# Kernel tuning notes

Measured on AMD Instinct MI355X. Metric: run time of the kernel, lower is better.

The kernel has to match this reference:

```python
import jax, jax.numpy as jnp
import numpy as np

B, T, V, E, H = 64, 512, 32000, 256, 512


def setup_inputs() -> dict:
    key = jax.random.key(0)
    k0, k1, k2, k3 = jax.random.split(key, 4)
    sequence_input = jax.random.randint(k0, (B, T), 0, V)
    emb_table = jax.random.normal(k1, (V, E), dtype=jnp.float32) * 0.02
    Wx = jax.random.normal(k2, (E, 4 * H), dtype=jnp.float32) * (1.0 / np.sqrt(E))
    Wh = jax.random.normal(k3, (H, 4 * H), dtype=jnp.float32) * (1.0 / np.sqrt(H))
    # Keras unit_forget_bias=True: forget-gate bias initialized to 1
    b = jnp.zeros((4 * H,), dtype=jnp.float32).at[H:2 * H].set(1.0)
    return {"sequence_input": sequence_input, "emb_table": emb_table,
            "Wx": Wx, "Wh": Wh, "b": b}


def _lstm(xz, Wh):
    # xz: [T, B, 4H] precomputed input projections (+bias); scan the recurrence.
    h0 = jnp.zeros((xz.shape[1], H), dtype=xz.dtype)
    c0 = jnp.zeros_like(h0)

    def step(carry, z_t):
        h, c = carry
        z = z_t + h @ Wh                      # [B, 4H]
        i, f, g, o = jnp.split(z, 4, axis=-1)  # Keras gate order: i, f, c(g), o
        i = jax.nn.sigmoid(i)
        f = jax.nn.sigmoid(f)
        g = jnp.tanh(g)
        o = jax.nn.sigmoid(o)
        c = f * c + i * g
        h = o * jnp.tanh(c)
        return (h, c), h

    (h_last, _c), seq = jax.lax.scan(step, (h0, c0), xz)
    return seq, h_last


def reference(sequence_input, emb_table, Wx, Wh, b):
    x = emb_table[sequence_input]                     # [B, T, E]
    xz = jnp.einsum('bte,eg->btg', x, Wx) + b         # [B, T, 4H]
    seq, h_last = _lstm(jnp.swapaxes(xz, 0, 1), Wh)   # seq: [T, B, H]
    seq = jnp.swapaxes(seq, 0, 1)                     # [B, T, H]
    mask = (sequence_input != 0).astype(jnp.float32)[..., None]  # [B, T, 1]
    return seq, h_last, mask
```

## Files before the change

kernel.cpp:

```cpp
#include <hip/hip_runtime.h>
#include <stdint.h>

#define B_   64
#define T_   512
#define E_   256
#define H_   512
#define G4_  2048
#define V_   32000

#define OUT_SEQ   0
#define OUT_HLAST 16777216
#define OUT_MASK  16809984

#define OFF_EMB  0u
#define OFF_WXT  16384000u
#define OFF_WHT  17432576u
#define OFF_C    19529728u
#define OFF_XZ   19660800u
#define XZ_PER_T   262144u
#define RING_PER_T  65536u
#define SLOT_U64    8192


#define POISON64 0xFFFFFFFFFFFFFFFFULL

typedef short bf16x8 __attribute__((ext_vector_type(8)));
typedef float f32x4  __attribute__((ext_vector_type(4)));
typedef unsigned int u32x4 __attribute__((ext_vector_type(4)));

__device__ __forceinline__ unsigned short f2bf(float f) {
  uint32_t u = __float_as_uint(f);
  u = (u + 0x7FFFu + ((u >> 16) & 1u)) >> 16;
  return (unsigned short)u;
}
__device__ __forceinline__ float bf2f(unsigned short h) {
  return __uint_as_float(((uint32_t)h) << 16);
}
__device__ __forceinline__ float sigmoid_f(float x) {
  return __fdividef(1.f, 1.f + __expf(-x));
}
__device__ __forceinline__ float tanh_f(float x) {
  return 1.f - __fdividef(2.f, 1.f + __expf(2.f * x));
}

__global__ void k_prep_emb(const float* __restrict__ emb, unsigned short* __restrict__ out) {
  int i = (blockIdx.x * 256 + threadIdx.x) * 4;
  if (i < V_ * E_) {
    float4 v = *(const float4*)(emb + i);
    ushort4 o;
    o.x = f2bf(v.x); o.y = f2bf(v.y); o.z = f2bf(v.z); o.w = f2bf(v.w);
    *(ushort4*)(out + i) = o;
  }
}

__global__ void k_prep_w(const float* __restrict__ Wx, const float* __restrict__ Wh,
                         unsigned short* __restrict__ wxt, unsigned short* __restrict__ wht) {
  int i = blockIdx.x * 256 + threadIdx.x;
  if (i < 524288) {
    int n = i >> 8, k = i & 255;
    wxt[i] = f2bf(Wx[k * G4_ + n]);
  } else if (i < 524288 + 1048576) {
    int j = i - 524288;
    int n = j >> 9, k = j & 511;
    wht[j] = f2bf(Wh[k * G4_ + n]);
  }
}

__global__ void k_mask(const int* __restrict__ seq, float* __restrict__ out) {
  int i = blockIdx.x * 256 + threadIdx.x;
  if (i < B_ * T_) out[OUT_MASK + i] = (seq[i] != 0) ? 1.f : 0.f;
}

__global__ __launch_bounds__(256) void k_copyseq(const unsigned int* __restrict__ ring,
                                                 float* __restrict__ out, int t0, int R) {
  int t = t0 + blockIdx.x;
  const unsigned int* src = ring + (size_t)(t % R) * (SLOT_U64 * 2);
  for (int i = threadIdx.x; i < B_ * H_ / 2; i += 256) {
    int b = i >> 8;
    int j = (i & 255) * 2;
    unsigned int v = src[((((b >> 4) * 64 + (j >> 3)) * 16 + (b & 15)) * 4) + ((j >> 1) & 3)];
    float2 o;
    o.x = bf2f((unsigned short)(v & 0xFFFFu));
    o.y = bf2f((unsigned short)(v >> 16));
    *(float2*)(out + ((size_t)b * T_ + t) * H_ + j) = o;
  }
}

__global__ void k_hlast(const unsigned int* __restrict__ ring, float* __restrict__ out, int R) {
  int i = blockIdx.x * 256 + threadIdx.x;
  if (i < B_ * H_) {
    int b = i >> 9, j = i & 511;
    unsigned int v = ring[(size_t)((T_ - 1) % R) * (SLOT_U64 * 2) +
                          ((((b >> 4) * 64 + (j >> 3)) * 16 + (b & 15)) * 4) + ((j >> 1) & 3)];
    out[OUT_HLAST + i] = bf2f((unsigned short)((j & 1) ? (v >> 16) : (v & 0xFFFFu)));
  }
}

#define LDA_ 264
__global__ __launch_bounds__(256) void k_gemm_xz(
    const int* __restrict__ seq, const unsigned short* __restrict__ embb,
    const unsigned short* __restrict__ wxt, const float* __restrict__ bias,
    unsigned short* __restrict__ xz, int t0) {
  __shared__ __align__(16) unsigned short a_lds[128 * LDA_];
  __shared__ __align__(16) unsigned short b_lds[128 * LDA_];
  int bx = blockIdx.x & 15;
  int by = blockIdx.x >> 4;
  int tid = threadIdx.x;

  {
    int r = tid >> 1, half = tid & 1;
    int m = by * 128 + r;
    int t = t0 + (m >> 6), b = m & 63;
    int idx = seq[b * T_ + t];
    const unsigned short* srcA = embb + (size_t)idx * E_ + half * 128;
    const unsigned short* srcB = wxt + (size_t)(bx * 128 + r) * E_ + half * 128;
    unsigned short* dstA = a_lds + r * LDA_ + half * 128;
    unsigned short* dstB = b_lds + r * LDA_ + half * 128;
#pragma unroll
    for (int q = 0; q < 16; ++q) {
      *(bf16x8*)(dstA + q * 8) = *(const bf16x8*)(srcA + q * 8);
      *(bf16x8*)(dstB + q * 8) = *(const bf16x8*)(srcB + q * 8);
    }
  }
  __syncthreads();

  int w = tid >> 6, lane = tid & 63;
  int l15 = lane & 15, l4 = lane >> 4;
  int wm = w >> 1, wn = w & 1;
  f32x4 acc[4][4] = {};
#pragma unroll
  for (int ks = 0; ks < 8; ++ks) {
    bf16x8 a[4], bb[4];
#pragma unroll
    for (int mf = 0; mf < 4; ++mf)
      a[mf] = *(const bf16x8*)(a_lds + (wm * 64 + mf * 16 + l15) * LDA_ + ks * 32 + 8 * l4);
#pragma unroll
    for (int nf = 0; nf < 4; ++nf)
      bb[nf] = *(const bf16x8*)(b_lds + (wn * 64 + nf * 16 + l15) * LDA_ + ks * 32 + 8 * l4);
#pragma unroll
    for (int mf = 0; mf < 4; ++mf)
#pragma unroll
      for (int nf = 0; nf < 4; ++nf)
        acc[mf][nf] = __builtin_amdgcn_mfma_f32_16x16x32_bf16(a[mf], bb[nf], acc[mf][nf], 0, 0, 0);
  }
#pragma unroll
  for (int nf = 0; nf < 4; ++nf) {
    int n = bx * 128 + wn * 64 + nf * 16 + l15;
    float bv = bias[n];
#pragma unroll
    for (int mf = 0; mf < 4; ++mf)
#pragma unroll
      for (int q = 0; q < 4; ++q) {
        int m = by * 128 + wm * 64 + mf * 16 + l4 * 4 + q;
        xz[(size_t)m * G4_ + n] = f2bf(acc[mf][nf][q] + bv);
      }
  }
}

__global__ __launch_bounds__(128, 1) void k_lstm(
    const unsigned short* __restrict__ wht, const unsigned short* __restrict__ xz,
    unsigned long long* hring, float* cbuf, int t0, int tend, int R) {
  int bid = blockIdx.x;
  int g = bid & 3, nwg = bid >> 2;
  int J0 = nwg * 32;
  int tid = threadIdx.x;
  int w = tid >> 6, lane = tid & 63;
  int l15 = lane & 15, l4 = lane >> 4;
  int bglob0 = g * 16;
  int jcol = J0 + w * 16 + l15;

  u32x4 Bs[4][16];
#pragma unroll
  for (int gt = 0; gt < 4; ++gt)
#pragma unroll
    for (int ks = 0; ks < 16; ++ks) {
      Bs[gt][ks] = *(const u32x4*)(wht + (size_t)(gt * 512 + jcol) * H_ + ks * 32 + l4 * 8);
      asm volatile("" : "+v"(Bs[gt][ks]));
    }

  float c4[4];
  if (t0 == 0) {
    c4[0] = c4[1] = c4[2] = c4[3] = 0.f;
  } else {
#pragma unroll
    for (int q = 0; q < 4; ++q) c4[q] = cbuf[(bglob0 + l4 * 4 + q) * H_ + jcol];
  }

  int kc   = nwg * 4 + w * 2 + (l15 >> 3);
  int half = (l15 >> 2) & 1;
  size_t pbase = ((size_t)(g * 64 + kc) * 16) * 2 + half;
  size_t rbase = (size_t)(g * 64 + l4) * 32 + l15 * 2;

  int xoff[16];
#pragma unroll
  for (int gt = 0; gt < 4; ++gt)
#pragma unroll
    for (int q = 0; q < 4; ++q)
      xoff[gt * 4 + q] = (l4 * 4 + q) * G4_ + gt * 512 + jcol;

  float xzf[16];
  {
    const unsigned short* x0 = xz + (size_t)bglob0 * G4_;
#pragma unroll
    for (int k = 0; k < 16; ++k) xzf[k] = bf2f(x0[xoff[k]]);
  }

  int t = t0;
  if (t0 == 0) {
    float hvf[4];
#pragma unroll
    for (int q = 0; q < 4; ++q) {
      float ig = sigmoid_f(xzf[0 * 4 + q]);
      float gg = tanh_f(xzf[2 * 4 + q]);
      float og = sigmoid_f(xzf[3 * 4 + q]);
      float cn = ig * gg;
      c4[q] = cn;
      hvf[q] = og * tanh_f(cn);
    }
    unsigned long long* hdst = hring;
#pragma unroll
    for (int q = 0; q < 4; ++q) {
      unsigned int my = f2bf(hvf[q]);
      unsigned int p1 = __shfl_xor(my, 1);
      unsigned int pair = my | (p1 << 16);
      unsigned int hi2 = __shfl_xor(pair, 2);
      if ((l15 & 3) == 0) {
        unsigned long long vv = (unsigned long long)pair | ((unsigned long long)hi2 << 32);
        __hip_atomic_store(&hdst[pbase + (size_t)(l4 * 4 + q) * 2], vv,
                           __ATOMIC_RELAXED, __HIP_MEMORY_SCOPE_AGENT);
      }
    }
    t = 1;
    if (t < tend) {
      const unsigned short* x1 = xz + ((size_t)1 * B_ + bglob0) * G4_;
#pragma unroll
      for (int k = 0; k < 16; ++k) xzf[k] = bf2f(x1[xoff[k]]);
    }
  }

  for (; t < tend; ++t) {
    f32x4 accA[4], accB[4];
#pragma unroll
    for (int gt = 0; gt < 4; ++gt)
#pragma unroll
      for (int q = 0; q < 4; ++q) { accA[gt][q] = xzf[gt * 4 + q]; accB[gt][q] = 0.f; }

    unsigned int raw[16];
    const unsigned short* xn = xz + ((size_t)(t + 1 - t0) * B_ + bglob0) * G4_;
    if (t + 1 < tend) {
#pragma unroll
      for (int k = 0; k < 16; ++k) raw[k] = xn[xoff[k]];
    }
    __builtin_amdgcn_sched_barrier(0);

    const unsigned long long* hsrc = hring + (size_t)((t - 1) % R) * SLOT_U64 + rbase;
    unsigned long long v[32];
    while (true) {
      bool ok = true;
#pragma unroll
      for (int ks = 0; ks < 16; ++ks) {
        v[2 * ks]     = __hip_atomic_load(hsrc + (size_t)ks * 128,     __ATOMIC_RELAXED, __HIP_MEMORY_SCOPE_AGENT);
        v[2 * ks + 1] = __hip_atomic_load(hsrc + (size_t)ks * 128 + 1, __ATOMIC_RELAXED, __HIP_MEMORY_SCOPE_AGENT);
      }
#pragma unroll
      for (int i = 0; i < 32; ++i) ok &= (v[i] != POISON64);
      if (__all(ok)) break;
      __builtin_amdgcn_s_sleep(1);
    }
    asm volatile("" ::: "memory");

#pragma unroll
    for (int ks = 0; ks < 16; ++ks) {
      union { unsigned long long u[2]; bf16x8 b; } cv;
      cv.u[0] = v[2 * ks]; cv.u[1] = v[2 * ks + 1];
      if (ks & 1) {
#pragma unroll
        for (int gt = 0; gt < 4; ++gt)
          accB[gt] = __builtin_amdgcn_mfma_f32_16x16x32_bf16(
              cv.b, __builtin_bit_cast(bf16x8, Bs[gt][ks]), accB[gt], 0, 0, 0);
      } else {
#pragma unroll
        for (int gt = 0; gt < 4; ++gt)
          accA[gt] = __builtin_amdgcn_mfma_f32_16x16x32_bf16(
              cv.b, __builtin_bit_cast(bf16x8, Bs[gt][ks]), accA[gt], 0, 0, 0);
      }
    }

    float hvf[4];
#pragma unroll
    for (int q = 0; q < 4; ++q) {
      float zi = accA[0][q] + accB[0][q];
      float zf = accA[1][q] + accB[1][q];
      float zg = accA[2][q] + accB[2][q];
      float zo = accA[3][q] + accB[3][q];
      float ig = sigmoid_f(zi);
      float fg = sigmoid_f(zf);
      float gg = tanh_f(zg);
      float og = sigmoid_f(zo);
      float cn = fg * c4[q] + ig * gg;
      c4[q] = cn;
      hvf[q] = og * tanh_f(cn);
    }

    unsigned long long* hdst = hring + (size_t)(t % R) * SLOT_U64;
#pragma unroll
    for (int q = 0; q < 4; ++q) {
      unsigned int my = f2bf(hvf[q]);
      unsigned int p1 = __shfl_xor(my, 1);
      unsigned int pair = my | (p1 << 16);
      unsigned int hi2 = __shfl_xor(pair, 2);
      if ((l15 & 3) == 0) {
        unsigned long long vv = (unsigned long long)pair | ((unsigned long long)hi2 << 32);
        __hip_atomic_store(&hdst[pbase + (size_t)(l4 * 4 + q) * 2], vv,
                           __ATOMIC_RELAXED, __HIP_MEMORY_SCOPE_AGENT);
      }
    }

    if (t + 1 < tend) {
#pragma unroll
      for (int k = 0; k < 16; ++k) xzf[k] = __uint_as_float(raw[k] << 16);
    }
  }

#pragma unroll
  for (int q = 0; q < 4; ++q) cbuf[(bglob0 + l4 * 4 + q) * H_ + jcol] = c4[q];
}

extern "C" void kernel_launch(void* const* d_in, const int* in_sizes, int n_in,
                              void* d_out, int out_size, void* d_ws, size_t ws_size,
                              hipStream_t stream) {
  const int* seq    = (const int*)d_in[0];
  const float* emb  = (const float*)d_in[1];
  const float* Wx   = (const float*)d_in[2];
  const float* Wh   = (const float*)d_in[3];
  const float* bias = (const float*)d_in[4];
  float* out = (float*)d_out;
  char* ws = (char*)d_ws;

  unsigned short* embb = (unsigned short*)(ws + OFF_EMB);
  unsigned short* wxt  = (unsigned short*)(ws + OFF_WXT);
  unsigned short* wht  = (unsigned short*)(ws + OFF_WHT);
  float* cbuf          = (float*)(ws + OFF_C);
  unsigned short* xz   = (unsigned short*)(ws + OFF_XZ);

  size_t cap = (ws_size > OFF_XZ) ? (ws_size - OFF_XZ) : 0;
  int TC = (cap > RING_PER_T) ? (int)((cap - RING_PER_T) / (XZ_PER_T + RING_PER_T)) : 2;
  if (TC > T_) TC = T_;
  TC &= ~1;
  if (TC < 2) TC = 2;
  int R = TC + 1;
  unsigned long long* hring = (unsigned long long*)(ws + OFF_XZ + (size_t)TC * XZ_PER_T);

  k_prep_emb<<<dim3(8000), dim3(256), 0, stream>>>(emb, embb);
  k_prep_w<<<dim3(6144), dim3(256), 0, stream>>>(Wx, Wh, wxt, wht);
  k_mask<<<dim3(128), dim3(256), 0, stream>>>(seq, out);

  for (int t0 = 0; t0 < T_; t0 += TC) {
    int tc = T_ - t0; if (tc > TC) tc = TC;
    int s0 = t0 % R;
    if (s0 + tc <= R) {
      hipMemsetAsync((char*)hring + (size_t)s0 * RING_PER_T, 0xFF, (size_t)tc * RING_PER_T, stream);
    } else {
      hipMemsetAsync((char*)hring + (size_t)s0 * RING_PER_T, 0xFF, (size_t)(R - s0) * RING_PER_T, stream);
      hipMemsetAsync((char*)hring, 0xFF, (size_t)(s0 + tc - R) * RING_PER_T, stream);
    }
    k_gemm_xz<<<dim3((tc / 2) * 16), dim3(256), 0, stream>>>(seq, embb, wxt, bias, xz, t0);
    k_lstm<<<dim3(64), dim3(128), 0, stream>>>(wht, xz, (unsigned long long*)hring, cbuf, t0, t0 + tc, R);
    k_copyseq<<<dim3(tc), dim3(256), 0, stream>>>((const unsigned int*)hring, out, t0, R);
  }
  k_hlast<<<dim3(128), dim3(256), 0, stream>>>((const unsigned int*)hring, out, R);
}
```

Measured before the change: 1.939 ms.

## Consume hidden-state chunks incrementally as they arrive instead of waiting for all

The spin-wait on the previous step's hidden-state ring is replaced by a per-chunk readiness mask. Each 32-element K-chunk is fed into the MFMA accumulation as soon as all lanes see it as non-poison, and only the missing chunks are reloaded. This lets matrix work overlap with waiting on slower producer workgroups instead of idling until the whole h vector is ready. It drops the split accA/accB accumulators in favour of a single chain, which lengthens the MFMA dependency chain, and it removes the s_sleep backoff, so polling traffic may rise.

```diff
diff --git a/kernel.cpp b/kernel.cpp
--- a/kernel.cpp
+++ b/kernel.cpp
@@ -186,9 +186,7 @@
     for (int q = 0; q < 4; ++q) c4[q] = cbuf[(bglob0 + l4 * 4 + q) * H_ + jcol];
   }
 
-  int kc   = nwg * 4 + w * 2 + (l15 >> 3);
-  int half = (l15 >> 2) & 1;
-  size_t pbase = ((size_t)(g * 64 + kc) * 16) * 2 + half;
+  size_t pbase = ((size_t)(g * 64 + (jcol >> 3)) * 16) * 2 + ((jcol >> 2) & 1);
   size_t rbase = (size_t)(g * 64 + l4) * 32 + l15 * 2;
 
   int xoff[16];
@@ -207,7 +205,7 @@
 
   int t = t0;
   if (t0 == 0) {
-    float hvf[4];
+    unsigned long long* hdst = hring;
 #pragma unroll
     for (int q = 0; q < 4; ++q) {
       float ig = sigmoid_f(xzf[0 * 4 + q]);
@@ -215,12 +213,8 @@
       float og = sigmoid_f(xzf[3 * 4 + q]);
       float cn = ig * gg;
       c4[q] = cn;
-      hvf[q] = og * tanh_f(cn);
-    }
-    unsigned long long* hdst = hring;
-#pragma unroll
-    for (int q = 0; q < 4; ++q) {
-      unsigned int my = f2bf(hvf[q]);
+      float hv = og * tanh_f(cn);
+      unsigned int my = f2bf(hv);
       unsigned int p1 = __shfl_xor(my, 1);
       unsigned int pair = my | (p1 << 16);
       unsigned int hi2 = __shfl_xor(pair, 2);
@@ -239,11 +233,19 @@
   }
 
   for (; t < tend; ++t) {
-    f32x4 accA[4], accB[4];
+    const unsigned long long* hsrc = hring + (size_t)((t - 1) % R) * SLOT_U64 + rbase;
+    unsigned long long v[32];
+#pragma unroll
+    for (int ks = 0; ks < 16; ++ks) {
+      v[2 * ks]     = __hip_atomic_load(hsrc + (size_t)ks * 128,     __ATOMIC_RELAXED, __HIP_MEMORY_SCOPE_AGENT);
+      v[2 * ks + 1] = __hip_atomic_load(hsrc + (size_t)ks * 128 + 1, __ATOMIC_RELAXED, __HIP_MEMORY_SCOPE_AGENT);
+    }
+
+    f32x4 acc[4];
 #pragma unroll
     for (int gt = 0; gt < 4; ++gt)
 #pragma unroll
-      for (int q = 0; q < 4; ++q) { accA[gt][q] = xzf[gt * 4 + q]; accB[gt][q] = 0.f; }
+      for (int q = 0; q < 4; ++q) acc[gt][q] = xzf[gt * 4 + q];
 
     unsigned int raw[16];
     const unsigned short* xn = xz + ((size_t)(t + 1 - t0) * B_ + bglob0) * G4_;
@@ -253,59 +255,45 @@
     }
     __builtin_amdgcn_sched_barrier(0);
 
-    const unsigned long long* hsrc = hring + (size_t)((t - 1) % R) * SLOT_U64 + rbase;
-    unsigned long long v[32];
-    while (true) {
-      bool ok = true;
+    unsigned dm = 0;
+    while (dm != 0xFFFFu) {
 #pragma unroll
       for (int ks = 0; ks < 16; ++ks) {
-        v[2 * ks]     = __hip_atomic_load(hsrc + (size_t)ks * 128,     __ATOMIC_RELAXED, __HIP_MEMORY_SCOPE_AGENT);
-        v[2 * ks + 1] = __hip_atomic_load(hsrc + (size_t)ks * 128 + 1, __ATOMIC_RELAXED, __HIP_MEMORY_SCOPE_AGENT);
-      }
-#pragma unroll
-      for (int i = 0; i < 32; ++i) ok &= (v[i] != POISON64);
-      if (__all(ok)) break;
-      __builtin_amdgcn_s_sleep(1);
+        if (!((dm >> ks) & 1u)) {
+          if (__all((v[2 * ks] != POISON64) & (v[2 * ks + 1] != POISON64))) {
+            union { unsigned long long u[2]; bf16x8 b; } cv;
+            cv.u[0] = v[2 * ks]; cv.u[1] = v[2 * ks + 1];
+#pragma unroll
+            for (int gt = 0; gt < 4; ++gt)
+              acc[gt] = __builtin_amdgcn_mfma_f32_16x16x32_bf16(
+                  cv.b, __builtin_bit_cast(bf16x8, Bs[gt][ks]), acc[gt], 0, 0, 0);
+            dm |= 1u << ks;
+          }
+        }
+      }
+      if (dm != 0xFFFFu) {
+#pragma unroll
+        for (int ks = 0; ks < 16; ++ks) {
+          if (!((dm >> ks) & 1u)) {
+            v[2 * ks]     = __hip_atomic_load(hsrc + (size_t)ks * 128,     __ATOMIC_RELAXED, __HIP_MEMORY_SCOPE_AGENT);
+            v[2 * ks + 1] = __hip_atomic_load(hsrc + (size_t)ks * 128 + 1, __ATOMIC_RELAXED, __HIP_MEMORY_SCOPE_AGENT);
+          }
+        }
+      }
     }
     asm volatile("" ::: "memory");
 
-#pragma unroll
-    for (int ks = 0; ks < 16; ++ks) {
-      union { unsigned long long u[2]; bf16x8 b; } cv;
-      cv.u[0] = v[2 * ks]; cv.u[1] = v[2 * ks + 1];
-      if (ks & 1) {
-#pragma unroll
-        for (int gt = 0; gt < 4; ++gt)
-          accB[gt] = __builtin_amdgcn_mfma_f32_16x16x32_bf16(
-              cv.b, __builtin_bit_cast(bf16x8, Bs[gt][ks]), accB[gt], 0, 0, 0);
-      } else {
-#pragma unroll
-        for (int gt = 0; gt < 4; ++gt)
-          accA[gt] = __builtin_amdgcn_mfma_f32_16x16x32_bf16(
-              cv.b, __builtin_bit_cast(bf16x8, Bs[gt][ks]), accA[gt], 0, 0, 0);
-      }
-    }
-
-    float hvf[4];
+    unsigned long long* hdst = hring + (size_t)(t % R) * SLOT_U64;
 #pragma unroll
     for (int q = 0; q < 4; ++q) {
-      float zi = accA[0][q] + accB[0][q];
-      float zf = accA[1][q] + accB[1][q];
-      float zg = accA[2][q] + accB[2][q];
-      float zo = accA[3][q] + accB[3][q];
-      float ig = sigmoid_f(zi);
-      float fg = sigmoid_f(zf);
-      float gg = tanh_f(zg);
-      float og = sigmoid_f(zo);
+      float ig = sigmoid_f(acc[0][q]);
+      float fg = sigmoid_f(acc[1][q]);
+      float gg = tanh_f(acc[2][q]);
+      float og = sigmoid_f(acc[3][q]);
       float cn = fg * c4[q] + ig * gg;
       c4[q] = cn;
-      hvf[q] = og * tanh_f(cn);
-    }
-
-    unsigned long long* hdst = hring + (size_t)(t % R) * SLOT_U64;
-#pragma unroll
-    for (int q = 0; q < 4; ++q) {
-      unsigned int my = f2bf(hvf[q]);
+      float hv = og * tanh_f(cn);
+      unsigned int my = f2bf(hv);
       unsigned int p1 = __shfl_xor(my, 1);
       unsigned int pair = my | (p1 << 16);
       unsigned int hi2 = __shfl_xor(pair, 2);
```

After: 2.677 ms. +38.1%, slower.

## Replace poison-polling on h ring with per-wave step counter flags

Applied to the files above, without the earlier changes.

The cross-workgroup handoff of the hidden state now uses per-wave monotonic step flags, replacing repeated polling of the full 32-value h payload for a poison sentinel. Each wave drains its stores with s_waitcnt and then publishes t+1 to its flag. Consumers spin on 32 flags per batch group and load h once those flags are ready. This drops the per-chunk memsets that re-poisoned the ring and cuts polling traffic. In exchange the flag store and data stores use only relaxed ordering with a waitcnt, which leaves a memory-visibility risk.

```diff
diff --git a/kernel.cpp b/kernel.cpp
--- a/kernel.cpp
+++ b/kernel.cpp
@@ -16,13 +16,12 @@
 #define OFF_WXT  16384000u
 #define OFF_WHT  17432576u
 #define OFF_C    19529728u
-#define OFF_XZ   19660800u
+#define OFF_FLAG 19660800u
+#define OFF_XZ   19664896u
 #define XZ_PER_T   262144u
 #define RING_PER_T  65536u
 #define SLOT_U64    8192
 
-
-#define POISON64 0xFFFFFFFFFFFFFFFFULL
 
 typedef short bf16x8 __attribute__((ext_vector_type(8)));
 typedef float f32x4  __attribute__((ext_vector_type(4)));
@@ -159,7 +158,8 @@
 
 __global__ __launch_bounds__(128, 1) void k_lstm(
     const unsigned short* __restrict__ wht, const unsigned short* __restrict__ xz,
-    unsigned long long* hring, float* cbuf, int t0, int tend, int R) {
+    unsigned long long* hring, float* cbuf, unsigned int* flags,
+    int t0, int tend, int R) {
   int bid = blockIdx.x;
   int g = bid & 3, nwg = bid >> 2;
   int J0 = nwg * 32;
@@ -186,10 +186,10 @@
     for (int q = 0; q < 4; ++q) c4[q] = cbuf[(bglob0 + l4 * 4 + q) * H_ + jcol];
   }
 
-  int kc   = nwg * 4 + w * 2 + (l15 >> 3);
-  int half = (l15 >> 2) & 1;
-  size_t pbase = ((size_t)(g * 64 + kc) * 16) * 2 + half;
+  size_t pbase = ((size_t)(g * 64 + (jcol >> 3)) * 16) * 2 + ((jcol >> 2) & 1);
   size_t rbase = (size_t)(g * 64 + l4) * 32 + l15 * 2;
+  unsigned int* myflag = flags + (g * 32 + nwg * 2 + w);
+  const unsigned int* gflags = flags + g * 32;
 
   int xoff[16];
 #pragma unroll
@@ -207,7 +207,7 @@
 
   int t = t0;
   if (t0 == 0) {
-    float hvf[4];
+    unsigned long long* hdst = hring;
 #pragma unroll
     for (int q = 0; q < 4; ++q) {
       float ig = sigmoid_f(xzf[0 * 4 + q]);
@@ -215,12 +215,8 @@
       float og = sigmoid_f(xzf[3 * 4 + q]);
       float cn = ig * gg;
       c4[q] = cn;
-      hvf[q] = og * tanh_f(cn);
-    }
-    unsigned long long* hdst = hring;
-#pragma unroll
-    for (int q = 0; q < 4; ++q) {
-      unsigned int my = f2bf(hvf[q]);
+      float hv = og * tanh_f(cn);
+      unsigned int my = f2bf(hv);
       unsigned int p1 = __shfl_xor(my, 1);
       unsigned int pair = my | (p1 << 16);
       unsigned int hi2 = __shfl_xor(pair, 2);
@@ -230,6 +226,9 @@
                            __ATOMIC_RELAXED, __HIP_MEMORY_SCOPE_AGENT);
       }
     }
+    asm volatile("s_waitcnt vmcnt(0)" ::: "memory");
+    if (lane == 0)
+      __hip_atomic_store(myflag, 1u, __ATOMIC_RELAXED, __HIP_MEMORY_SCOPE_AGENT);
     t = 1;
     if (t < tend) {
       const unsigned short* x1 = xz + ((size_t)1 * B_ + bglob0) * G4_;
@@ -239,12 +238,6 @@
   }
 
   for (; t < tend; ++t) {
-    f32x4 accA[4], accB[4];
-#pragma unroll
-    for (int gt = 0; gt < 4; ++gt)
-#pragma unroll
-      for (int q = 0; q < 4; ++q) { accA[gt][q] = xzf[gt * 4 + q]; accB[gt][q] = 0.f; }
-
     unsigned int raw[16];
     const unsigned short* xn = xz + ((size_t)(t + 1 - t0) * B_ + bglob0) * G4_;
     if (t + 1 < tend) {
@@ -253,21 +246,30 @@
     }
     __builtin_amdgcn_sched_barrier(0);
 
+    {
+      unsigned int need = (unsigned int)t;
+      while (true) {
+        unsigned int fv = __hip_atomic_load(gflags + (lane & 31),
+                                            __ATOMIC_RELAXED, __HIP_MEMORY_SCOPE_AGENT);
+        if (__all(fv >= need)) break;
+      }
+    }
+    asm volatile("" ::: "memory");
+    __builtin_amdgcn_sched_barrier(0);
+
     const unsigned long long* hsrc = hring + (size_t)((t - 1) % R) * SLOT_U64 + rbase;
     unsigned long long v[32];
-    while (true) {
-      bool ok = true;
-#pragma unroll
-      for (int ks = 0; ks < 16; ++ks) {
-        v[2 * ks]     = __hip_atomic_load(hsrc + (size_t)ks * 128,     __ATOMIC_RELAXED, __HIP_MEMORY_SCOPE_AGENT);
-        v[2 * ks + 1] = __hip_atomic_load(hsrc + (size_t)ks * 128 + 1, __ATOMIC_RELAXED, __HIP_MEMORY_SCOPE_AGENT);
-      }
-#pragma unroll
-      for (int i = 0; i < 32; ++i) ok &= (v[i] != POISON64);
-      if (__all(ok)) break;
-      __builtin_amdgcn_s_sleep(1);
-    }
-    asm volatile("" ::: "memory");
+#pragma unroll
+    for (int ks = 0; ks < 16; ++ks) {
+      v[2 * ks]     = __hip_atomic_load(hsrc + (size_t)ks * 128,     __ATOMIC_RELAXED, __HIP_MEMORY_SCOPE_AGENT);
+      v[2 * ks + 1] = __hip_atomic_load(hsrc + (size_t)ks * 128 + 1, __ATOMIC_RELAXED, __HIP_MEMORY_SCOPE_AGENT);
+    }
+
+    f32x4 accA[4], accB[4];
+#pragma unroll
+    for (int gt = 0; gt < 4; ++gt)
+#pragma unroll
+      for (int q = 0; q < 4; ++q) { accA[gt][q] = xzf[gt * 4 + q]; accB[gt][q] = 0.f; }
 
 #pragma unroll
     for (int ks = 0; ks < 16; ++ks) {
@@ -286,7 +288,7 @@
       }
     }
 
-    float hvf[4];
+    unsigned long long* hdst = hring + (size_t)(t % R) * SLOT_U64;
 #pragma unroll
     for (int q = 0; q < 4; ++q) {
       float zi = accA[0][q] + accB[0][q];
@@ -299,13 +301,8 @@
       float og = sigmoid_f(zo);
       float cn = fg * c4[q] + ig * gg;
       c4[q] = cn;
-      hvf[q] = og * tanh_f(cn);
-    }
-
-    unsigned long long* hdst = hring + (size_t)(t % R) * SLOT_U64;
-#pragma unroll
-    for (int q = 0; q < 4; ++q) {
-      unsigned int my = f2bf(hvf[q]);
+      float hv = og * tanh_f(cn);
+      unsigned int my = f2bf(hv);
       unsigned int p1 = __shfl_xor(my, 1);
       unsigned int pair = my | (p1 << 16);
       unsigned int hi2 = __shfl_xor(pair, 2);
@@ -315,6 +312,10 @@
                            __ATOMIC_RELAXED, __HIP_MEMORY_SCOPE_AGENT);
       }
     }
+    asm volatile("s_waitcnt vmcnt(0)" ::: "memory");
+    if (lane == 0)
+      __hip_atomic_store(myflag, (unsigned int)(t + 1),
+                         __ATOMIC_RELAXED, __HIP_MEMORY_SCOPE_AGENT);
 
     if (t + 1 < tend) {
 #pragma unroll
@@ -341,6 +342,7 @@
   unsigned short* wxt  = (unsigned short*)(ws + OFF_WXT);
   unsigned short* wht  = (unsigned short*)(ws + OFF_WHT);
   float* cbuf          = (float*)(ws + OFF_C);
+  unsigned int* flags  = (unsigned int*)(ws + OFF_FLAG);
   unsigned short* xz   = (unsigned short*)(ws + OFF_XZ);
 
   size_t cap = (ws_size > OFF_XZ) ? (ws_size - OFF_XZ) : 0;
@@ -351,21 +353,16 @@
   int R = TC + 1;
   unsigned long long* hring = (unsigned long long*)(ws + OFF_XZ + (size_t)TC * XZ_PER_T);
 
+  hipMemsetAsync(flags, 0, 512, stream);
   k_prep_emb<<<dim3(8000), dim3(256), 0, stream>>>(emb, embb);
   k_prep_w<<<dim3(6144), dim3(256), 0, stream>>>(Wx, Wh, wxt, wht);
   k_mask<<<dim3(128), dim3(256), 0, stream>>>(seq, out);
 
   for (int t0 = 0; t0 < T_; t0 += TC) {
     int tc = T_ - t0; if (tc > TC) tc = TC;
-    int s0 = t0 % R;
-    if (s0 + tc <= R) {
-      hipMemsetAsync((char*)hring + (size_t)s0 * RING_PER_T, 0xFF, (size_t)tc * RING_PER_T, stream);
-    } else {
-      hipMemsetAsync((char*)hring + (size_t)s0 * RING_PER_T, 0xFF, (size_t)(R - s0) * RING_PER_T, stream);
-      hipMemsetAsync((char*)hring, 0xFF, (size_t)(s0 + tc - R) * RING_PER_T, stream);
-    }
     k_gemm_xz<<<dim3((tc / 2) * 16), dim3(256), 0, stream>>>(seq, embb, wxt, bias, xz, t0);
-    k_lstm<<<dim3(64), dim3(128), 0, stream>>>(wht, xz, (unsigned long long*)hring, cbuf, t0, t0 + tc, R);
+    k_lstm<<<dim3(64), dim3(128), 0, stream>>>(wht, xz, (unsigned long long*)hring, cbuf,
+                                               flags, t0, t0 + tc, R);
     k_copyseq<<<dim3(tc), dim3(256), 0, stream>>>((const unsigned int*)hring, out, t0, R);
   }
   k_hlast<<<dim3(128), dim3(256), 0, stream>>>((const unsigned int*)hring, out, R);
```

After: 2.706 ms. 39.6% more time.
